# Kernel tuning notes

Hardware: AMD Instinct MI355X
Metric: run time of the kernel (lower is better)

The kernel has to match this reference:

```python
import jax, jax.numpy as jnp
import numpy as np

DIM = 384
HEADS = 12
WIN = (7, 7)
N = WIN[0] * WIN[1]  # 49 tokens per window
B = 2048             # total windows
NW = 64              # windows per image (mask groups)


def _relative_position_index():
    ch, cw = np.meshgrid(np.arange(WIN[0]), np.arange(WIN[1]), indexing='ij')
    coords = np.stack([ch, cw]).reshape(2, -1)                 # [2, N]
    rel = coords[:, :, None] - coords[:, None, :]              # [2, N, N]
    rel = rel.transpose(1, 2, 0)                               # [N, N, 2]
    rel[..., 0] += WIN[0] - 1
    rel[..., 1] += WIN[1] - 1
    rel[..., 0] *= 2 * WIN[1] - 1
    return rel.sum(-1).astype(np.int32)                        # [N, N]


def setup_inputs() -> dict:
    key = jax.random.key(0)
    ks = jax.random.split(key, 7)
    table_sz = (2 * WIN[0] - 1) * (2 * WIN[1] - 1)             # 169
    return {
        'x': jax.random.normal(ks[0], (B, N, DIM), jnp.float32),
        'mask': jax.random.normal(ks[1], (NW, N, N), jnp.float32),
        'qkv_w': jax.random.normal(ks[2], (3 * DIM, DIM), jnp.float32) * (DIM ** -0.5),
        'qkv_b': jnp.zeros((3 * DIM,), jnp.float32),
        'proj_w': jax.random.normal(ks[3], (DIM, DIM), jnp.float32) * (DIM ** -0.5),
        'proj_b': jnp.zeros((DIM,), jnp.float32),
        'rel_table': jax.random.normal(ks[4], (table_sz, HEADS), jnp.float32) * 0.02,
        'rel_index': jnp.asarray(_relative_position_index()),
    }


def reference(x, mask, qkv_w, qkv_b, proj_w, proj_b, rel_table, rel_index):
    b, n, c = x.shape
    h, hd = HEADS, c // HEADS
    scale = hd ** -0.5
    qkv = (x @ qkv_w.T + qkv_b).reshape(b, n, 3, h, hd)
    q, k, v = (qkv[:, :, 0].transpose(0, 2, 1, 3),
               qkv[:, :, 1].transpose(0, 2, 1, 3),
               qkv[:, :, 2].transpose(0, 2, 1, 3))             # [b, h, n, hd]
    attn = jnp.einsum('bhid,bhjd->bhij', q * scale, k)         # [b, h, n, n]
    bias = rel_table[rel_index.reshape(-1)].reshape(n, n, h).transpose(2, 0, 1)
    attn = attn + bias[None]
    nw = mask.shape[0]
    attn = attn.reshape(b // nw, nw, h, n, n) + mask[None, :, None]
    attn = jax.nn.softmax(attn.reshape(b, h, n, n), axis=-1)
    out = jnp.einsum('bhij,bhjd->bihd', attn, v).reshape(b, n, c)
    return out @ proj_w.T + proj_b
```

## Files before the change

### kernel.cpp

```cpp
#include <hip/hip_runtime.h>

#define DIM   384
#define HEADS 12
#define NTOK  49
#define NWIN  2048
#define NMASK 64
#define HD    32
#define MTOT  (NWIN * NTOK)

typedef __bf16 bf16x8 __attribute__((ext_vector_type(8)));
typedef float  floatx4 __attribute__((ext_vector_type(4)));

__device__ __forceinline__ unsigned short f2bf(float f) {
  unsigned int u = __builtin_bit_cast(unsigned int, f);
  u += 0x7fffu + ((u >> 16) & 1u);
  return (unsigned short)(u >> 16);
}
__device__ __forceinline__ uint4 cvt8(float4 a, float4 b) {
  uint4 r;
  r.x = (unsigned)f2bf(a.x) | ((unsigned)f2bf(a.y) << 16);
  r.y = (unsigned)f2bf(a.z) | ((unsigned)f2bf(a.w) << 16);
  r.z = (unsigned)f2bf(b.x) | ((unsigned)f2bf(b.y) << 16);
  r.w = (unsigned)f2bf(b.z) | ((unsigned)f2bf(b.w) << 16);
  return r;
}
__device__ __forceinline__ void async_copy16(const void* g, void* l) {
  __builtin_amdgcn_global_load_lds((const __attribute__((address_space(1))) void*)g,
                                   (__attribute__((address_space(3))) void*)l, 16, 0, 0);
}

__global__ void prep_kernel(const float* __restrict__ qkv_w,
                            const float* __restrict__ proj_w,
                            const float* __restrict__ rel_table,
                            const int*   __restrict__ rel_index,
                            const float* __restrict__ mask,
                            unsigned short* __restrict__ qkv_wb,
                            unsigned short* __restrict__ proj_wb,
                            float* __restrict__ biasP,
                            float* __restrict__ maskP) {
  const int tid  = blockIdx.x * blockDim.x + threadIdx.x;
  const int nthr = gridDim.x * blockDim.x;

  const int nw4 = (3 * DIM * DIM) / 4;
  for (int i = tid; i < nw4; i += nthr) {
    float4 v = ((const float4*)qkv_w)[i];
    ushort4 o = { f2bf(v.x), f2bf(v.y), f2bf(v.z), f2bf(v.w) };
    ((ushort4*)qkv_wb)[i] = o;
  }
  const int np4 = (DIM * DIM) / 4;
  for (int i = tid; i < np4; i += nthr) {
    float4 v = ((const float4*)proj_w)[i];
    ushort4 o = { f2bf(v.x), f2bf(v.y), f2bf(v.z), f2bf(v.w) };
    ((ushort4*)proj_wb)[i] = o;
  }
  for (int i = tid; i < 12288; i += nthr) {
    const int lane = i & 63;
    const int t    = (i >> 6) & 15;
    const int h    = i >> 10;
    const int rb   = (t >> 2) * 16 + (lane >> 4) * 4;
    const int c    = (t & 3) * 16 + (lane & 15);
    float4 o;
    float* op = (float*)&o;
#pragma unroll
    for (int reg = 0; reg < 4; reg++) {
      const int r = rb + reg;
      op[reg] = (r < NTOK && c < NTOK)
                  ? rel_table[rel_index[r * NTOK + c] * HEADS + h]
                  : -1e30f;
    }
    ((float4*)biasP)[i] = o;
  }
  for (int i = tid; i < 65536; i += nthr) {
    const int lane = i & 63;
    const int t    = (i >> 6) & 15;
    const int g    = i >> 10;
    const int rb   = (t >> 2) * 16 + (lane >> 4) * 4;
    const int c    = (t & 3) * 16 + (lane & 15);
    float4 o;
    float* op = (float*)&o;
#pragma unroll
    for (int reg = 0; reg < 4; reg++) {
      const int r = rb + reg;
      op[reg] = (r < NTOK && c < NTOK)
                  ? mask[g * (NTOK * NTOK) + r * NTOK + c]
                  : -1e30f;
    }
    ((float4*)maskP)[i] = o;
  }
}

template <int OUT_BF16, int A_FP32>
__global__ __launch_bounds__(256, 2)
void gemm_bt(const void* __restrict__ Ap,
             const unsigned short* __restrict__ W,
             const float* __restrict__ bias,
             void* __restrict__ Cout,
             int M, int N, int K) {
  constexpr int ESTR = OUT_BF16 ? 144 : 272;
  constexpr int ESZ  = 16 * ESTR;
  __shared__ __align__(16) char lds[OUT_BF16 ? (4 * 2 * 16 * 144)
                                             : (4 * 2 * 16 * 272)];
  char* ldsA = lds;
  char* ldsB = lds + 8192;

  const int tid  = threadIdx.x;
  const int lane = tid & 63;
  const int wave = tid >> 6;
  const int wr   = wave >> 1;
  const int wc   = wave & 1;
  const int q4   = lane >> 4;
  const int lm   = lane & 15;

  const int NT  = N >> 7;
  const int cpx = gridDim.x >> 3;
  const int lin = (blockIdx.x & 7) * cpx + (blockIdx.x >> 3);
  const int tileM = (lin / NT) * 128;
  const int tileN = (lin % NT) * 128;

  const int srow = tid >> 2;
  const int scol = (tid & 3) * 8;
  const unsigned short* gA = nullptr;
  const float*          gAf = nullptr;
  if constexpr (A_FP32)
    gAf = (const float*)Ap + (size_t)(tileM + srow) * K + scol;
  else
    gA = (const unsigned short*)Ap + (size_t)(tileM + srow) * K + scol;
  const unsigned short* gB = W + (size_t)(tileN + srow) * K + scol;
  const int loff = tid * 16;

  const int aoff = (wr * 64 + lm) * 64 + q4 * 16;
  const int boff = (wc * 64 + lm) * 64 + q4 * 16;

  float4 pa0, pa1, pa2, pa3;
  if constexpr (A_FP32) {
    pa0 = *(const float4*)(gAf);
    pa1 = *(const float4*)(gAf + 4);
    pa2 = *(const float4*)(gAf + (size_t)64 * K);
    pa3 = *(const float4*)(gAf + (size_t)64 * K + 4);
    gAf += 32;
  }

  floatx4 acc[4][4] = {};

  for (int k0 = 0; k0 < K; k0 += 32) {
    if constexpr (A_FP32) {
      *(uint4*)(ldsA + loff)        = cvt8(pa0, pa1);
      *(uint4*)(ldsA + 4096 + loff) = cvt8(pa2, pa3);
    } else {
      async_copy16(gA,          ldsA + loff);
      async_copy16(gA + 64 * K, ldsA + 4096 + loff);
      gA += 32;
    }
    async_copy16(gB,          ldsB + loff);
    async_copy16(gB + 64 * K, ldsB + 4096 + loff);
    gB += 32;
    __syncthreads();

    if constexpr (A_FP32) {
      if (k0 + 32 < K) {
        pa0 = *(const float4*)(gAf);
        pa1 = *(const float4*)(gAf + 4);
        pa2 = *(const float4*)(gAf + (size_t)64 * K);
        pa3 = *(const float4*)(gAf + (size_t)64 * K + 4);
        gAf += 32;
      }
    }

    bf16x8 af[4], bfr[4];
#pragma unroll
    for (int i = 0; i < 4; i++) {
      af[i]  = *(const bf16x8*)(ldsA + aoff + i * 1024);
      bfr[i] = *(const bf16x8*)(ldsB + boff + i * 1024);
    }
#pragma unroll
    for (int i = 0; i < 4; i++)
#pragma unroll
      for (int j = 0; j < 4; j++)
        acc[i][j] = __builtin_amdgcn_mfma_f32_16x16x32_bf16(af[i], bfr[j], acc[i][j], 0, 0, 0);
    __syncthreads();
  }

  float bvj[4];
#pragma unroll
  for (int j = 0; j < 4; j++) bvj[j] = bias[tileN + wc * 64 + j * 16 + lm];

  char* Eb = lds + wave * (2 * ESZ);
#pragma unroll
  for (int i = 0; i < 4; i++) {
    char* Ep = Eb + (i & 1) * ESZ;
    if (OUT_BF16) {
#pragma unroll
      for (int j = 0; j < 4; j++)
#pragma unroll
        for (int r = 0; r < 4; r++)
          *(unsigned short*)(Ep + (q4 * 4 + r) * 144 + (j * 16 + lm) * 2) =
              f2bf(acc[i][j][r] + bvj[j]);
#pragma unroll
      for (int it = 0; it < 2; it++) {
        const int c   = lane + it * 64;
        const int row = c >> 3;
        const int c8  = c & 7;
        const uint4 v = *(const uint4*)(Ep + row * 144 + c8 * 16);
        unsigned short* dst = (unsigned short*)Cout +
            (size_t)(tileM + wr * 64 + i * 16 + row) * N + tileN + wc * 64 + c8 * 8;
        *(uint4*)dst = v;
      }
    } else {
#pragma unroll
      for (int j = 0; j < 4; j++)
#pragma unroll
        for (int r = 0; r < 4; r++)
          *(float*)(Ep + (q4 * 4 + r) * 272 + (j * 16 + lm) * 4) =
              acc[i][j][r] + bvj[j];
#pragma unroll
      for (int it = 0; it < 4; it++) {
        const int c   = lane + it * 64;
        const int row = c >> 4;
        const int c4  = c & 15;
        const uint4 v = *(const uint4*)(Ep + row * 272 + c4 * 16);
        float* dst = (float*)Cout +
            (size_t)(tileM + wr * 64 + i * 16 + row) * N + tileN + wc * 64 + c4 * 4;
        *(uint4*)dst = v;
      }
    }
  }
}

__global__ __launch_bounds__(256, 8)
void attn_mfma(const unsigned short* __restrict__ qkv,
               const float* __restrict__ biasP,
               const float* __restrict__ maskP,
               unsigned short* __restrict__ attn_out) {
  __shared__ __align__(16) char lds[16128];
  char* Vt = lds;
  char* Qb = lds + 6912;
  char* Kb = lds + 11008;
  char* Pb = lds + 6912;

  const int tid  = threadIdx.x;
  const int wave = tid >> 6;
  const int lane = tid & 63;
  const int lm   = lane & 15;
  const int q    = lane >> 4;

  const int pair = (blockIdx.x & 7) * (NWIN * HEADS / 8) + (blockIdx.x >> 3);
  const int b    = pair / HEADS;
  const int h    = pair - b * HEADS;
  const int g    = b & (NMASK - 1);

  const unsigned short* qbase = qkv + (size_t)b * NTOK * (3 * DIM) + h * HD;

  {
    const int row   = tid >> 2;
    const int chunk = tid & 3;
    uint4 vq = {0u, 0u, 0u, 0u}, vk = vq;
    if (row < NTOK) {
      vq = *(const uint4*)(qbase + (size_t)row * (3 * DIM) + chunk * 8);
      vk = *(const uint4*)(qbase + (size_t)row * (3 * DIM) + DIM + chunk * 8);
    }
    *(uint4*)(Qb + row * 64 + chunk * 16) = vq;
    *(uint4*)(Kb + row * 64 + chunk * 16) = vk;
  }
  {
    const int tok = tid >> 2;
    const int c   = tid & 3;
    uint4 vv = {0u, 0u, 0u, 0u};
    if (tok < NTOK) vv = *(const uint4*)(qbase + 2 * DIM + (size_t)tok * (3 * DIM) + c * 8);
    const unsigned short* e = (const unsigned short*)&vv;
#pragma unroll
    for (int j = 0; j < 8; j++)
      *(unsigned short*)(Vt + (c * 8 + j) * 144 + tok * 2) = e[j];
    if (tid < 64)
      *(unsigned short*)(Vt + HD * 144 + tid * 2) =
          (tid < NTOK) ? (unsigned short)0x3F80 : (unsigned short)0;
  }
  __syncthreads();

  bf16x8 qf, kf[4];
  qf = *(const bf16x8*)(Qb + (wave * 16 + lm) * 64 + q * 16);
#pragma unroll
  for (int j = 0; j < 4; j++)
    kf[j] = *(const bf16x8*)(Kb + (j * 16 + lm) * 64 + q * 16);
  floatx4 S[4] = {};
#pragma unroll
  for (int j = 0; j < 4; j++)
    S[j] = __builtin_amdgcn_mfma_f32_16x16x32_bf16(qf, kf[j], S[j], 0, 0, 0);

  __syncthreads();

  const float scale = 0.17677669529663687f;
  const float* bb = biasP + (size_t)h * 4096;
  const float* mm = maskP + (size_t)g * 4096;
#pragma unroll
  for (int j = 0; j < 4; j++) {
    const int t = wave * 4 + j;
    const float4 b4 = ((const float4*)bb)[t * 64 + lane];
    const float4 m4 = ((const float4*)mm)[t * 64 + lane];
    const float* bp = (const float*)&b4;
    const float* mp = (const float*)&m4;
#pragma unroll
    for (int r = 0; r < 4; r++) {
      const float s = fmaf(S[j][r], scale, bp[r] + mp[r]);
      const float p = __expf(s);
      *(unsigned short*)(Pb + (wave * 16 + q * 4 + r) * 144 + (j * 16 + lm) * 2) = f2bf(p);
    }
  }

  floatx4 O[3] = {};
#pragma unroll
  for (int ks = 0; ks < 2; ks++) {
    const bf16x8 pf = *(const bf16x8*)(Pb + (wave * 16 + lm) * 144 + ks * 64 + q * 16);
#pragma unroll
    for (int n = 0; n < 3; n++) {
      const bf16x8 vf = *(const bf16x8*)(Vt + (n * 16 + lm) * 144 + ks * 64 + q * 16);
      O[n] = __builtin_amdgcn_mfma_f32_16x16x32_bf16(pf, vf, O[n], 0, 0, 0);
    }
  }

  unsigned short* obase = attn_out + (size_t)b * NTOK * DIM + h * HD;
#pragma unroll
  for (int r = 0; r < 4; r++) {
    const float sv  = __shfl(O[2][r], lane & 48, 64);
    const float inv = __builtin_amdgcn_rcpf(sv);
    const int row = wave * 16 + q * 4 + r;
    if (row < NTOK) {
#pragma unroll
      for (int n = 0; n < 2; n++)
        obase[(size_t)row * DIM + n * 16 + lm] = f2bf(O[n][r] * inv);
    }
  }
}

extern "C" void kernel_launch(void* const* d_in, const int* in_sizes, int n_in,
                              void* d_out, int out_size, void* d_ws, size_t ws_size,
                              hipStream_t stream) {
  const float* x         = (const float*)d_in[0];
  const float* mask      = (const float*)d_in[1];
  const float* qkv_w     = (const float*)d_in[2];
  const float* qkv_b     = (const float*)d_in[3];
  const float* proj_w    = (const float*)d_in[4];
  const float* proj_b    = (const float*)d_in[5];
  const float* rel_table = (const float*)d_in[6];
  const int*   rel_index = (const int*)d_in[7];
  float* out = (float*)d_out;

  char* ws = (char*)d_ws;
  unsigned short* attn_o  = (unsigned short*)(ws);
  unsigned short* qkvbuf  = (unsigned short*)(ws + 77070336);
  unsigned short* qkv_wb  = (unsigned short*)(ws + 308281344);
  unsigned short* proj_wb = (unsigned short*)(ws + 309166080);
  float*          biasP   = (float*)(ws + 309460992);
  float*          maskP   = (float*)(ws + 309657600);

  prep_kernel<<<768, 256, 0, stream>>>(qkv_w, proj_w, rel_table, rel_index,
                                       mask, qkv_wb, proj_wb, biasP, maskP);

  gemm_bt<1, 1><<<dim3((MTOT / 128) * ((3 * DIM) / 128)), 256, 0, stream>>>(
      x, qkv_wb, qkv_b, qkvbuf, MTOT, 3 * DIM, DIM);

  attn_mfma<<<dim3(NWIN * HEADS), 256, 0, stream>>>(qkvbuf, biasP, maskP,
                                                    attn_o);

  gemm_bt<0, 0><<<dim3((MTOT / 128) * (DIM / 128)), 256, 0, stream>>>(
      attn_o, proj_wb, proj_b, out, MTOT, DIM, DIM);
}
```

Measured before the change: 542.6 us.

## Double-buffer LDS tiles in GEMM main loop and use native bf16 conversion

Splits the GEMM shared-memory staging into two A and two B buffers so the next K-slice is loaded (async to LDS, or via registers for fp32 A) while MFMAs run on the current slice. This cuts the per-iteration barriers from two to one and overlaps global latency with compute. The cvt8 helper now uses compiler __bf16 casts instead of manual bit rounding, which may map to hardware conversion instructions. The LDS footprint grows to 32 KB, which could limit occupancy under the 2-blocks-per-SM launch bound.

```diff
diff --git a/kernel.cpp b/kernel.cpp
--- a/kernel.cpp
+++ b/kernel.cpp
@@ -17,12 +17,12 @@
   return (unsigned short)(u >> 16);
 }
 __device__ __forceinline__ uint4 cvt8(float4 a, float4 b) {
-  uint4 r;
-  r.x = (unsigned)f2bf(a.x) | ((unsigned)f2bf(a.y) << 16);
-  r.y = (unsigned)f2bf(a.z) | ((unsigned)f2bf(a.w) << 16);
-  r.z = (unsigned)f2bf(b.x) | ((unsigned)f2bf(b.y) << 16);
-  r.w = (unsigned)f2bf(b.z) | ((unsigned)f2bf(b.w) << 16);
-  return r;
+  union { uint4 u; __bf16 h[8]; } r;
+  r.h[0] = (__bf16)a.x; r.h[1] = (__bf16)a.y;
+  r.h[2] = (__bf16)a.z; r.h[3] = (__bf16)a.w;
+  r.h[4] = (__bf16)b.x; r.h[5] = (__bf16)b.y;
+  r.h[6] = (__bf16)b.z; r.h[7] = (__bf16)b.w;
+  return r.u;
 }
 __device__ __forceinline__ void async_copy16(const void* g, void* l) {
   __builtin_amdgcn_global_load_lds((const __attribute__((address_space(1))) void*)g,
@@ -98,10 +98,9 @@
              int M, int N, int K) {
   constexpr int ESTR = OUT_BF16 ? 144 : 272;
   constexpr int ESZ  = 16 * ESTR;
-  __shared__ __align__(16) char lds[OUT_BF16 ? (4 * 2 * 16 * 144)
-                                             : (4 * 2 * 16 * 272)];
-  char* ldsA = lds;
-  char* ldsB = lds + 8192;
+  constexpr int LDS_MAIN = 32768;
+  constexpr int LDS_EPI  = 4 * 2 * ESZ;
+  __shared__ __align__(16) char lds[(LDS_MAIN > LDS_EPI) ? LDS_MAIN : LDS_EPI];
 
   const int tid  = threadIdx.x;
   const int lane = tid & 63;
@@ -131,53 +130,73 @@
   const int aoff = (wr * 64 + lm) * 64 + q4 * 16;
   const int boff = (wc * 64 + lm) * 64 + q4 * 16;
 
+  char* curA = lds;
+  char* nxtA = lds + 8192;
+  char* curB = lds + 16384;
+  char* nxtB = lds + 24576;
+
+  floatx4 acc[4][4] = {};
   float4 pa0, pa1, pa2, pa3;
+
   if constexpr (A_FP32) {
     pa0 = *(const float4*)(gAf);
     pa1 = *(const float4*)(gAf + 4);
     pa2 = *(const float4*)(gAf + (size_t)64 * K);
     pa3 = *(const float4*)(gAf + (size_t)64 * K + 4);
     gAf += 32;
-  }
-
-  floatx4 acc[4][4] = {};
+    *(uint4*)(curA + loff)        = cvt8(pa0, pa1);
+    *(uint4*)(curA + 4096 + loff) = cvt8(pa2, pa3);
+  } else {
+    async_copy16(gA,          curA + loff);
+    async_copy16(gA + 64 * K, curA + 4096 + loff);
+    gA += 32;
+  }
+  async_copy16(gB,          curB + loff);
+  async_copy16(gB + 64 * K, curB + 4096 + loff);
+  gB += 32;
+  __syncthreads();
 
   for (int k0 = 0; k0 < K; k0 += 32) {
-    if constexpr (A_FP32) {
-      *(uint4*)(ldsA + loff)        = cvt8(pa0, pa1);
-      *(uint4*)(ldsA + 4096 + loff) = cvt8(pa2, pa3);
-    } else {
-      async_copy16(gA,          ldsA + loff);
-      async_copy16(gA + 64 * K, ldsA + 4096 + loff);
-      gA += 32;
-    }
-    async_copy16(gB,          ldsB + loff);
-    async_copy16(gB + 64 * K, ldsB + 4096 + loff);
-    gB += 32;
-    __syncthreads();
-
-    if constexpr (A_FP32) {
-      if (k0 + 32 < K) {
+    const bool pref = (k0 + 32 < K);
+    if (pref) {
+      if constexpr (A_FP32) {
         pa0 = *(const float4*)(gAf);
         pa1 = *(const float4*)(gAf + 4);
         pa2 = *(const float4*)(gAf + (size_t)64 * K);
         pa3 = *(const float4*)(gAf + (size_t)64 * K + 4);
         gAf += 32;
+      } else {
+        async_copy16(gA,          nxtA + loff);
+        async_copy16(gA + 64 * K, nxtA + 4096 + loff);
+        gA += 32;
       }
+      async_copy16(gB,          nxtB + loff);
+      async_copy16(gB + 64 * K, nxtB + 4096 + loff);
+      gB += 32;
     }
 
     bf16x8 af[4], bfr[4];
 #pragma unroll
     for (int i = 0; i < 4; i++) {
-      af[i]  = *(const bf16x8*)(ldsA + aoff + i * 1024);
-      bfr[i] = *(const bf16x8*)(ldsB + boff + i * 1024);
+      af[i]  = *(const bf16x8*)(curA + aoff + i * 1024);
+      bfr[i] = *(const bf16x8*)(curB + boff + i * 1024);
     }
 #pragma unroll
     for (int i = 0; i < 4; i++)
 #pragma unroll
       for (int j = 0; j < 4; j++)
         acc[i][j] = __builtin_amdgcn_mfma_f32_16x16x32_bf16(af[i], bfr[j], acc[i][j], 0, 0, 0);
+
+    if constexpr (A_FP32) {
+      if (pref) {
+        *(uint4*)(nxtA + loff)        = cvt8(pa0, pa1);
+        *(uint4*)(nxtA + 4096 + loff) = cvt8(pa2, pa3);
+      }
+    }
     __syncthreads();
+    char* t;
+    t = curA; curA = nxtA; nxtA = t;
+    t = curB; curB = nxtB; nxtB = t;
   }
 
   float bvj[4];
```

Result: slower. 565.7 us (+4.3%).

## Stage fp32 A tiles into LDS via async copies with XOR swizzle, convert on read

Applied to the files above, without the earlier changes.

For the fp32-input GEMM, the A tile is now loaded straight into LDS as fp32 with global_load_lds async copies using an XOR-swizzled layout, instead of loading to registers, converting to bf16 and storing. Conversion to bf16 happens after the LDS read, once per fragment, using native casts. This removes the register prefetch and the VGPR-to-LDS store path, but doubles the LDS footprint for A and the LDS read traffic. The fp32 A data is no longer prefetched ahead of the barrier.

```diff
diff --git a/kernel.cpp b/kernel.cpp
--- a/kernel.cpp
+++ b/kernel.cpp
@@ -16,12 +16,10 @@
   u += 0x7fffu + ((u >> 16) & 1u);
   return (unsigned short)(u >> 16);
 }
-__device__ __forceinline__ uint4 cvt8(float4 a, float4 b) {
-  uint4 r;
-  r.x = (unsigned)f2bf(a.x) | ((unsigned)f2bf(a.y) << 16);
-  r.y = (unsigned)f2bf(a.z) | ((unsigned)f2bf(a.w) << 16);
-  r.z = (unsigned)f2bf(b.x) | ((unsigned)f2bf(b.y) << 16);
-  r.w = (unsigned)f2bf(b.z) | ((unsigned)f2bf(b.w) << 16);
+__device__ __forceinline__ bf16x8 cvt8f(float4 a, float4 b) {
+  bf16x8 r;
+  r[0] = (__bf16)a.x; r[1] = (__bf16)a.y; r[2] = (__bf16)a.z; r[3] = (__bf16)a.w;
+  r[4] = (__bf16)b.x; r[5] = (__bf16)b.y; r[6] = (__bf16)b.z; r[7] = (__bf16)b.w;
   return r;
 }
 __device__ __forceinline__ void async_copy16(const void* g, void* l) {
@@ -98,10 +96,12 @@
              int M, int N, int K) {
   constexpr int ESTR = OUT_BF16 ? 144 : 272;
   constexpr int ESZ  = 16 * ESTR;
-  __shared__ __align__(16) char lds[OUT_BF16 ? (4 * 2 * 16 * 144)
-                                             : (4 * 2 * 16 * 272)];
+  constexpr int ABYTES   = A_FP32 ? 16384 : 8192;
+  constexpr int LDS_MAIN = ABYTES + 8192;
+  constexpr int LDS_EPI  = 4 * 2 * ESZ;
+  __shared__ __align__(16) char lds[(LDS_MAIN > LDS_EPI) ? LDS_MAIN : LDS_EPI];
   char* ldsA = lds;
-  char* ldsB = lds + 8192;
+  char* ldsB = lds + ABYTES;
 
   const int tid  = threadIdx.x;
   const int lane = tid & 63;
@@ -120,32 +120,32 @@
   const int srow = tid >> 2;
   const int scol = (tid & 3) * 8;
   const unsigned short* gA = nullptr;
-  const float*          gAf = nullptr;
-  if constexpr (A_FP32)
-    gAf = (const float*)Ap + (size_t)(tileM + srow) * K + scol;
-  else
+  const float* gac[4];
+  if constexpr (A_FP32) {
+#pragma unroll
+    for (int c = 0; c < 4; c++) {
+      const int s   = c * 256 + tid;
+      const int row = s >> 3;
+      const int gg  = (s & 7) ^ (row & 7);
+      gac[c] = (const float*)Ap + (size_t)(tileM + row) * K + gg * 4;
+    }
+  } else {
     gA = (const unsigned short*)Ap + (size_t)(tileM + srow) * K + scol;
+  }
   const unsigned short* gB = W + (size_t)(tileN + srow) * K + scol;
   const int loff = tid * 16;
 
   const int aoff = (wr * 64 + lm) * 64 + q4 * 16;
   const int boff = (wc * 64 + lm) * 64 + q4 * 16;
-
-  float4 pa0, pa1, pa2, pa3;
-  if constexpr (A_FP32) {
-    pa0 = *(const float4*)(gAf);
-    pa1 = *(const float4*)(gAf + 4);
-    pa2 = *(const float4*)(gAf + (size_t)64 * K);
-    pa3 = *(const float4*)(gAf + (size_t)64 * K + 4);
-    gAf += 32;
-  }
+  const int x7   = lm & 7;
 
   floatx4 acc[4][4] = {};
 
   for (int k0 = 0; k0 < K; k0 += 32) {
     if constexpr (A_FP32) {
-      *(uint4*)(ldsA + loff)        = cvt8(pa0, pa1);
-      *(uint4*)(ldsA + 4096 + loff) = cvt8(pa2, pa3);
+#pragma unroll
+      for (int c = 0; c < 4; c++)
+        async_copy16(gac[c] + k0, ldsA + c * 4096 + loff);
     } else {
       async_copy16(gA,          ldsA + loff);
       async_copy16(gA + 64 * K, ldsA + 4096 + loff);
@@ -156,20 +156,17 @@
     gB += 32;
     __syncthreads();
 
-    if constexpr (A_FP32) {
-      if (k0 + 32 < K) {
-        pa0 = *(const float4*)(gAf);
-        pa1 = *(const float4*)(gAf + 4);
-        pa2 = *(const float4*)(gAf + (size_t)64 * K);
-        pa3 = *(const float4*)(gAf + (size_t)64 * K + 4);
-        gAf += 32;
+    bf16x8 af[4], bfr[4];
+#pragma unroll
+    for (int i = 0; i < 4; i++) {
+      if constexpr (A_FP32) {
+        const int r = wr * 64 + i * 16 + lm;
+        const float4 fa = *(const float4*)(ldsA + r * 128 + (((2 * q4)    ) ^ x7) * 16);
+        const float4 fb = *(const float4*)(ldsA + r * 128 + (((2 * q4) | 1) ^ x7) * 16);
+        af[i] = cvt8f(fa, fb);
+      } else {
+        af[i] = *(const bf16x8*)(ldsA + aoff + i * 1024);
       }
-    }
-
-    bf16x8 af[4], bfr[4];
-#pragma unroll
-    for (int i = 0; i < 4; i++) {
-      af[i]  = *(const bf16x8*)(ldsA + aoff + i * 1024);
       bfr[i] = *(const bf16x8*)(ldsB + boff + i * 1024);
     }
 #pragma unroll
```

After: 542.3 us. About the same (-0.0%).
